# Kernel optimization log

Measured on AMD Instinct MI355X. Metric: run time of the kernel, lower is better.

## Reference

```python
import jax, jax.numpy as jnp
import numpy as np

NHEAD = 4
HEAD_DIM = 64  # att_features per head = atten_feats // nhead


def setup_inputs() -> dict:
    key = jax.random.key(0)
    ks = jax.random.split(key, 8)
    N, D = 8192, 256
    s = 1.0 / np.sqrt(D)
    return {
        "x": jax.random.normal(ks[0], (N, D), dtype=jnp.float32),
        "edge": jax.random.randint(ks[1], (N, N), 0, 2, dtype=jnp.int32),
        "Wq": jax.random.normal(ks[2], (D, D), dtype=jnp.float32) * s,
        "bq": jax.random.normal(ks[3], (D,), dtype=jnp.float32) * 0.01,
        "Wk": jax.random.normal(ks[4], (D, D), dtype=jnp.float32) * s,
        "bk": jax.random.normal(ks[5], (D,), dtype=jnp.float32) * 0.01,
        "Wv": jax.random.normal(ks[6], (D, D), dtype=jnp.float32) * s,
        "bv": jax.random.normal(ks[7], (D,), dtype=jnp.float32) * 0.01,
    }


def _split_heads(t):
    # (N, H*d) -> (H, N, d)
    N = t.shape[0]
    return t.reshape(N, NHEAD, HEAD_DIM).transpose(1, 0, 2)


def reference(x, edge, Wq, bq, Wk, bk, Wv, bv):
    q = _split_heads(x @ Wq + bq)  # (H, N, d)
    k = _split_heads(x @ Wk + bk)
    v = _split_heads(x @ Wv + bv)
    # additive graph mask: 0 where edge.T == 1, -10000 where edge.T == 0
    mask = (edge.T.astype(jnp.float32) - 1.0) * 10000.0  # (N, N)
    scores = jnp.einsum("hnd,hmd->hnm", q, k) / np.sqrt(HEAD_DIM)
    scores = scores + mask[None, :, :]
    attn = jax.nn.softmax(scores, axis=-1)  # dropout is identity at eval
    ctx = jnp.einsum("hnm,hmd->hnd", attn, v)
    # (H, N, d) -> (N, H*d)
    return ctx.transpose(1, 0, 2).reshape(x.shape[0], NHEAD * HEAD_DIM)
```

## Files before the change

### kernel.cpp

```cpp
#include <hip/hip_runtime.h>
#include <stdint.h>

typedef unsigned short u16;
typedef unsigned int u32;
typedef unsigned long long u64;

typedef __attribute__((ext_vector_type(8))) __bf16 bf16x8;
typedef __attribute__((ext_vector_type(4))) float f32x4;

#define NROW 8192
#define DMODEL 256
#define HD 64
#define LDT 72

__device__ __forceinline__ u16 f2bf(float f) {
    u32 u = __builtin_bit_cast(u32, f);
    u += 0x7FFFu + ((u >> 16) & 1u);
    return (u16)(u >> 16);
}
__device__ __forceinline__ bf16x8 ldb8(const u16* p) {
    uint4 v = *(const uint4*)p;
    return __builtin_bit_cast(bf16x8, v);
}
__device__ __forceinline__ f32x4 mfma16(bf16x8 a, bf16x8 b, f32x4 c) {
    return __builtin_amdgcn_mfma_f32_16x16x32_bf16(a, b, c, 0, 0, 0);
}

__global__ __launch_bounds__(256) void k_prep(
    const float* __restrict__ x,
    const float* __restrict__ Wq, const float* __restrict__ Wk,
    const float* __restrict__ Wv,
    u16* __restrict__ xb, u16* __restrict__ Wt) {
    const int t = threadIdx.x;
    if (blockIdx.x < 1024) {
        size_t idx = (size_t)blockIdx.x * 2048 + t * 8;
        f32x4 a = *(const f32x4*)&x[idx];
        f32x4 b = *(const f32x4*)&x[idx + 4];
        uint4 o;
        o.x = (u32)f2bf(a[0]) | ((u32)f2bf(a[1]) << 16);
        o.y = (u32)f2bf(a[2]) | ((u32)f2bf(a[3]) << 16);
        o.z = (u32)f2bf(b[0]) | ((u32)f2bf(b[1]) << 16);
        o.w = (u32)f2bf(b[2]) | ((u32)f2bf(b[3]) << 16);
        *(uint4*)&xb[idx] = o;
        return;
    }
    __shared__ __align__(16) u16 lw[64 * LDT];
    int wb = blockIdx.x - 1024;
    int mat = wb >> 4, tile = wb & 15;
    int k0 = (tile >> 2) * 64, n0 = (tile & 3) * 64;
    const float* W = (mat == 0) ? Wq : ((mat == 1) ? Wk : Wv);
    #pragma unroll
    for (int i = 0; i < 4; ++i) {
        int c = t + 256 * i;
        int k = c >> 4, c4 = c & 15;
        f32x4 w4 = *(const f32x4*)&W[(size_t)(k0 + k) * DMODEL + n0 + c4 * 4];
        uint2 pk;
        pk.x = (u32)f2bf(w4[0]) | ((u32)f2bf(w4[1]) << 16);
        pk.y = (u32)f2bf(w4[2]) | ((u32)f2bf(w4[3]) << 16);
        *(uint2*)&lw[k * LDT + c4 * 4] = pk;
    }
    __syncthreads();
    #pragma unroll
    for (int i = 0; i < 2; ++i) {
        int c = t + 256 * i;
        int n = c >> 3, k8 = c & 7;
        union { uint4 u; u16 s[8]; } pk;
        #pragma unroll
        for (int j = 0; j < 8; ++j) pk.s[j] = lw[(k8 * 8 + j) * LDT + n];
        *(uint4*)&Wt[(size_t)mat * 65536 + (size_t)(n0 + n) * DMODEL + k0 + k8 * 8] = pk.u;
    }
}

__global__ __launch_bounds__(256) void k_bitmask(const int* __restrict__ edge,
                                                 u64* __restrict__ bits) {
    __shared__ u64 lb[8][128];
    const int t = threadIdx.x;
    const int lane = t & 63, w = t >> 6;
    const u32 m8 = blockIdx.x * 8u;
    #pragma unroll
    for (int rr = 0; rr < 2; ++rr) {
        const int mloc = w * 2 + rr;
        const size_t base = (size_t)(m8 + mloc) * NROW;
        for (int nwb = 0; nwb < 128; nwb += 16) {
            int v[16];
            #pragma unroll
            for (int j = 0; j < 16; ++j)
                v[j] = edge[base + (size_t)(nwb + j) * 64 + lane];
            u64 b[16];
            #pragma unroll
            for (int j = 0; j < 16; ++j) b[j] = __ballot(v[j] != 0);
            if (lane == 0) {
                #pragma unroll
                for (int j = 0; j < 16; ++j) lb[mloc][nwb + j] = b[j];
            }
        }
    }
    __syncthreads();
    const int nw = t >> 1, mh = (t & 1) * 4;
    u64 a0 = lb[mh + 0][nw], a1 = lb[mh + 1][nw];
    u64 a2 = lb[mh + 2][nw], a3 = lb[mh + 3][nw];
    u64* dst = &bits[(size_t)nw * NROW + m8 + mh];
    uint4 p0, p1;
    p0.x = (u32)a0; p0.y = (u32)(a0 >> 32); p0.z = (u32)a1; p0.w = (u32)(a1 >> 32);
    p1.x = (u32)a2; p1.y = (u32)(a2 >> 32); p1.z = (u32)a3; p1.w = (u32)(a3 >> 32);
    *(uint4*)dst = p0;
    *(uint4*)(dst + 2) = p1;
}

__global__ __launch_bounds__(256, 3) void k_qkv(
    const u16* __restrict__ xb, const u16* __restrict__ Wt,
    const float* __restrict__ bq, const float* __restrict__ bk,
    const float* __restrict__ bv,
    u16* __restrict__ Qo, u16* __restrict__ Ko, u16* __restrict__ Vt) {
    __shared__ __align__(16) u16 ax[128 * LDT];
    __shared__ __align__(16) u16 wt[64 * LDT];
    const int t = threadIdx.x;
    const int lane = t & 63, wv = t >> 6;
    const int q4 = lane >> 4, l15 = lane & 15;
    const int wr = wv >> 1, wc = wv & 1;
    const int row0 = blockIdx.x * 128;
    const int mat = blockIdx.y >> 2;
    const int c0 = (blockIdx.y & 3) * 64;
    const u16* Wm = Wt + (size_t)mat * 65536;
    const float* bias = (mat == 0) ? bq : ((mat == 1) ? bk : bv);

    f32x4 acc[8];
    #pragma unroll
    for (int i = 0; i < 8; ++i) acc[i] = {0.f, 0.f, 0.f, 0.f};

    for (int kk = 0; kk < DMODEL; kk += 64) {
        #pragma unroll
        for (int i = 0; i < 4; ++i) {
            int c = t + 256 * i;
            int row = c >> 3, c8 = c & 7;
            *(uint4*)&ax[row * LDT + c8 * 8] =
                *(const uint4*)&xb[(size_t)(row0 + row) * DMODEL + kk + c8 * 8];
        }
        #pragma unroll
        for (int i = 0; i < 2; ++i) {
            int c = t + 256 * i;
            int n = c >> 3, c8 = c & 7;
            *(uint4*)&wt[n * LDT + c8 * 8] =
                *(const uint4*)&Wm[(size_t)(c0 + n) * DMODEL + kk + c8 * 8];
        }
        __syncthreads();
        #pragma unroll
        for (int ks = 0; ks < 2; ++ks) {
            bf16x8 xf[4], wf[2];
            #pragma unroll
            for (int it = 0; it < 4; ++it)
                xf[it] = ldb8(&ax[(wr * 64 + it * 16 + l15) * LDT + ks * 32 + q4 * 8]);
            #pragma unroll
            for (int jt = 0; jt < 2; ++jt)
                wf[jt] = ldb8(&wt[(wc * 32 + jt * 16 + l15) * LDT + ks * 32 + q4 * 8]);
            if (mat < 2) {
                #pragma unroll
                for (int it = 0; it < 4; ++it)
                    #pragma unroll
                    for (int jt = 0; jt < 2; ++jt)
                        acc[it * 2 + jt] = mfma16(xf[it], wf[jt], acc[it * 2 + jt]);
            } else {
                #pragma unroll
                for (int jt = 0; jt < 2; ++jt)
                    #pragma unroll
                    for (int it = 0; it < 4; ++it)
                        acc[jt * 4 + it] = mfma16(wf[jt], xf[it], acc[jt * 4 + it]);
            }
        }
        __syncthreads();
    }

    if (mat < 2) {
        u16* out = (mat == 0) ? Qo : Ko;
        const float scale = (mat == 0) ? 0.18033688f : 1.0f;
        #pragma unroll
        for (int jt = 0; jt < 2; ++jt) {
            int col = c0 + wc * 32 + jt * 16 + l15;
            float bcol = bias[col];
            #pragma unroll
            for (int it = 0; it < 4; ++it) {
                int rowb = row0 + wr * 64 + it * 16 + q4 * 4;
                f32x4 a = acc[it * 2 + jt];
                #pragma unroll
                for (int r = 0; r < 4; ++r)
                    out[(size_t)(rowb + r) * DMODEL + col] = f2bf((a[r] + bcol) * scale);
            }
        }
    } else {
        #pragma unroll
        for (int jt = 0; jt < 2; ++jt) {
            #pragma unroll
            for (int r = 0; r < 4; ++r) {
                int drow = c0 + wc * 32 + jt * 16 + q4 * 4 + r;
                float bd = bias[drow];
                #pragma unroll
                for (int it = 0; it < 4; ++it) {
                    int col = row0 + wr * 64 + it * 16 + l15;
                    Vt[(size_t)drow * NROW + col] = f2bf(acc[jt * 4 + it][r] + bd);
                }
            }
        }
    }
}

__global__ __launch_bounds__(256, 3) void k_attn(
    const u16* __restrict__ Q, const u16* __restrict__ K,
    const u16* __restrict__ Vt, const u64* __restrict__ bits,
    float* __restrict__ po) {
    __shared__ __align__(16) u16 sK[2][64 * 64];
    __shared__ __align__(16) u16 sV[2][64 * 64];
    __shared__ __align__(16) u16 sP[4][32 * 64];
    __shared__ __align__(16) u32 sB[2][2][2][64];

    const int t = threadIdx.x;
    const int lane = t & 63, w = t >> 6;
    const int q4 = lane >> 4, l15 = lane & 15;
    const int l7 = l15 & 7;
    const int bid = blockIdx.x;
    const int sl = bid >> 8;
    const int b8 = bid & 255;
    const int h = b8 & 3;
    const int qt = b8 >> 2;
    const int n0 = qt * 128;
    const int mbase = sl * 2048;
    const int half = w >> 1;
    const u32 shift = (u32)((w & 1) * 16 + l15);
    const int sr = t >> 3, sc = t & 7;
    const int ssw = (sc ^ (sr & 7)) * 8;
    const int bg = t >> 6, bm = t & 63;

    bf16x8 qf[2][2];
    #pragma unroll
    for (int nt = 0; nt < 2; ++nt)
        #pragma unroll
        for (int ks = 0; ks < 2; ++ks)
            qf[nt][ks] = ldb8(&Q[(size_t)(n0 + nt * 64 + w * 16 + l15) * DMODEL +
                                 h * HD + ks * 32 + q4 * 8]);

    uint4 onesu = {0x3F803F80u, 0x3F803F80u, 0x3F803F80u, 0x3F803F80u};
    const bf16x8 ones = __builtin_bit_cast(bf16x8, onesu);

    f32x4 o[2][4], lacc[2];
    #pragma unroll
    for (int nt = 0; nt < 2; ++nt) {
        lacc[nt] = {0.f, 0.f, 0.f, 0.f};
        #pragma unroll
        for (int dt = 0; dt < 4; ++dt) o[nt][dt] = {0.f, 0.f, 0.f, 0.f};
    }

    uint4 rk0, rk1, rv0, rv1; uint2 rb;
    {
        rk0 = *(const uint4*)&K[(size_t)(mbase + sr) * DMODEL + h * HD + sc * 8];
        rk1 = *(const uint4*)&K[(size_t)(mbase + 32 + sr) * DMODEL + h * HD + sc * 8];
        rv0 = *(const uint4*)&Vt[(size_t)(h * HD + sr) * NROW + mbase + sc * 8];
        rv1 = *(const uint4*)&Vt[(size_t)(h * HD + 32 + sr) * NROW + mbase + sc * 8];
        if (t < 128) rb = *(const uint2*)&bits[(size_t)(qt * 2 + bg) * NROW + mbase + bm];
        *(uint4*)&sK[0][sr * 64 + ssw] = rk0;
        *(uint4*)&sK[0][(32 + sr) * 64 + ssw] = rk1;
        *(uint4*)&sV[0][sr * 64 + ssw] = rv0;
        *(uint4*)&sV[0][(32 + sr) * 64 + ssw] = rv1;
        if (t < 128) { sB[0][bg][0][bm] = rb.x; sB[0][bg][1][bm] = rb.y; }
    }

    for (int it = 0; it < 32; ++it) {
        __syncthreads();
        const int buf = it & 1;
        if (it < 31) {
            int m0 = mbase + (it + 1) * 64;
            rk0 = *(const uint4*)&K[(size_t)(m0 + sr) * DMODEL + h * HD + sc * 8];
            rk1 = *(const uint4*)&K[(size_t)(m0 + 32 + sr) * DMODEL + h * HD + sc * 8];
            rv0 = *(const uint4*)&Vt[(size_t)(h * HD + sr) * NROW + m0 + sc * 8];
            rv1 = *(const uint4*)&Vt[(size_t)(h * HD + 32 + sr) * NROW + m0 + sc * 8];
            if (t < 128) rb = *(const uint2*)&bits[(size_t)(qt * 2 + bg) * NROW + m0 + bm];
        }

        f32x4 s[2][4];
        #pragma unroll
        for (int nt = 0; nt < 2; ++nt)
            #pragma unroll
            for (int tj = 0; tj < 4; ++tj) s[nt][tj] = {0.f, 0.f, 0.f, 0.f};
        #pragma unroll
        for (int ks = 0; ks < 2; ++ks) {
            bf16x8 kb[4];
            #pragma unroll
            for (int tj = 0; tj < 4; ++tj)
                kb[tj] = ldb8(&sK[buf][(tj * 16 + l15) * 64 + (((ks * 4 + q4) ^ l7) * 8)]);
            #pragma unroll
            for (int nt = 0; nt < 2; ++nt)
                #pragma unroll
                for (int tj = 0; tj < 4; ++tj)
                    s[nt][tj] = mfma16(kb[tj], qf[nt][ks], s[nt][tj]);
        }

        #pragma unroll
        for (int nt = 0; nt < 2; ++nt) {
            #pragma unroll
            for (int tj = 0; tj < 4; ++tj) {
                uint4 bw = *(const uint4*)&sB[buf][nt][half][tj * 16 + q4 * 4];
                u32 wd[4] = {bw.x, bw.y, bw.z, bw.w};
                u32 ub[4];
                #pragma unroll
                for (int r = 0; r < 4; ++r) {
                    float sv = ((wd[r] >> shift) & 1u) ? s[nt][tj][r] : -1e30f;
                    ub[r] = __builtin_bit_cast(u32, __builtin_amdgcn_exp2f(sv));
                }
                uint2 pk;
                pk.x = (ub[0] >> 16) | (ub[1] & 0xFFFF0000u);
                pk.y = (ub[2] >> 16) | (ub[3] & 0xFFFF0000u);
                *(uint2*)&sP[w][(nt * 16 + l15) * 64 +
                                (((tj * 2 + (q4 >> 1)) ^ l7) * 8) + (q4 & 1) * 4] = pk;
            }
        }
        asm volatile("s_waitcnt lgkmcnt(0)" ::: "memory");

        #pragma unroll
        for (int ks = 0; ks < 2; ++ks) {
            bf16x8 pf[2], vb[4];
            #pragma unroll
            for (int nt = 0; nt < 2; ++nt)
                pf[nt] = ldb8(&sP[w][(nt * 16 + l15) * 64 + (((ks * 4 + q4) ^ l7) * 8)]);
            #pragma unroll
            for (int dt = 0; dt < 4; ++dt)
                vb[dt] = ldb8(&sV[buf][(dt * 16 + l15) * 64 + (((ks * 4 + q4) ^ l7) * 8)]);
            #pragma unroll
            for (int nt = 0; nt < 2; ++nt) {
                #pragma unroll
                for (int dt = 0; dt < 4; ++dt)
                    o[nt][dt] = mfma16(pf[nt], vb[dt], o[nt][dt]);
                lacc[nt] = mfma16(pf[nt], ones, lacc[nt]);
            }
        }

        if (it < 31) {
            const int nb = buf ^ 1;
            *(uint4*)&sK[nb][sr * 64 + ssw] = rk0;
            *(uint4*)&sK[nb][(32 + sr) * 64 + ssw] = rk1;
            *(uint4*)&sV[nb][sr * 64 + ssw] = rv0;
            *(uint4*)&sV[nb][(32 + sr) * 64 + ssw] = rv1;
            if (t < 128) { sB[nb][bg][0][bm] = rb.x; sB[nb][bg][1][bm] = rb.y; }
        }
    }

    float* pob = po + (size_t)bid * 8320;
    #pragma unroll
    for (int nt = 0; nt < 2; ++nt)
        #pragma unroll
        for (int dt = 0; dt < 4; ++dt)
            *(f32x4*)&pob[(dt * 16 + l15) * 128 + nt * 64 + w * 16 + q4 * 4] = o[nt][dt];
    if (l15 == 0) {
        #pragma unroll
        for (int nt = 0; nt < 2; ++nt)
            #pragma unroll
            for (int r = 0; r < 4; ++r)
                pob[8192 + nt * 64 + w * 16 + q4 * 4 + r] = lacc[nt][r];
    }
}

__global__ __launch_bounds__(256) void k_reduce(const float* __restrict__ po,
                                                float* __restrict__ out) {
    __shared__ float sT[64 * 132];
    __shared__ float sL[128];
    const int t = threadIdx.x;
    const int b8 = blockIdx.x;
    const int h = b8 & 3;
    const int qt = b8 >> 2;
    const int n0 = qt * 128;
    const size_t base = (size_t)b8 * 8320;
    const int d = t >> 2, ng = (t & 3) * 32;
    f32x4 a[8];
    #pragma unroll
    for (int j = 0; j < 8; ++j) a[j] = {0.f, 0.f, 0.f, 0.f};
    #pragma unroll
    for (int s = 0; s < 4; ++s) {
        const float* p = po + base + (size_t)s * (256 * 8320) + d * 128 + ng;
        #pragma unroll
        for (int j = 0; j < 8; ++j) a[j] += *(const f32x4*)&p[j * 4];
    }
    #pragma unroll
    for (int j = 0; j < 8; ++j) *(f32x4*)&sT[d * 132 + ng + j * 4] = a[j];
    if (t < 128) {
        float l = 0.f;
        #pragma unroll
        for (int s = 0; s < 4; ++s) l += po[base + (size_t)s * (256 * 8320) + 8192 + t];
        sL[t] = l;
    }
    __syncthreads();
    const int n = t >> 1, dg = (t & 1) * 32;
    float inv = __builtin_amdgcn_rcpf(sL[n] + 1e-30f);
    #pragma unroll
    for (int j = 0; j < 8; ++j) {
        f32x4 v;
        #pragma unroll
        for (int i = 0; i < 4; ++i) v[i] = sT[(dg + j * 4 + i) * 132 + n];
        v = v * inv;
        *(f32x4*)&out[(size_t)(n0 + n) * DMODEL + h * HD + dg + j * 4] = v;
    }
}

extern "C" void kernel_launch(void* const* d_in, const int* in_sizes, int n_in,
                              void* d_out, int out_size, void* d_ws, size_t ws_size,
                              hipStream_t stream) {
    const float* x  = (const float*)d_in[0];
    const int* edge = (const int*)d_in[1];
    const float* Wq = (const float*)d_in[2];
    const float* bq = (const float*)d_in[3];
    const float* Wk = (const float*)d_in[4];
    const float* bk = (const float*)d_in[5];
    const float* Wv = (const float*)d_in[6];
    const float* bv = (const float*)d_in[7];

    char* ws = (char*)d_ws;
    u64* bits = (u64*)ws;
    u16* Qo  = (u16*)(ws + (8u << 20));
    u16* Ko  = (u16*)(ws + (12u << 20));
    u16* Vt  = (u16*)(ws + (16u << 20));
    u16* xb  = (u16*)(ws + (20u << 20));
    u16* Wt  = (u16*)(ws + (24u << 20));
    float* po = (float*)(ws + (32u << 20));
    float* out = (float*)d_out;

    hipLaunchKernelGGL(k_prep, dim3(1072), dim3(256), 0, stream, x, Wq, Wk, Wv, xb, Wt);
    hipLaunchKernelGGL(k_bitmask, dim3(1024), dim3(256), 0, stream, edge, bits);
    hipLaunchKernelGGL(k_qkv, dim3(64, 12), dim3(256), 0, stream,
                       xb, Wt, bq, bk, bv, Qo, Ko, Vt);
    hipLaunchKernelGGL(k_attn, dim3(1024), dim3(256), 0, stream, Qo, Ko, Vt, bits, po);
    hipLaunchKernelGGL(k_reduce, dim3(256), dim3(256), 0, stream, po, out);
}
```

Baseline: 503.4 us.

## Merge bitmask into QKV kernel and double attention query tile to 256 rows

The edge-bitmask kernel and the QKV projection kernel are merged into one launch, with the first 1024 blocks building the mask and the rest doing the GEMM, so the two independent jobs can overlap. The attention kernel now processes 256 query rows per block instead of 128, which halves the number of blocks and the re-reads of each K/V tile, and registers, LDS and partial-output size grow to match. Occupancy bound drops to 2 blocks per CU, and the grid falls to 512 blocks on a 256-CU part, which risks lower latency hiding and poorer load balance.

```diff
diff --git a/kernel.cpp b/kernel.cpp
--- a/kernel.cpp
+++ b/kernel.cpp
@@ -71,56 +71,58 @@
     }
 }
 
-__global__ __launch_bounds__(256) void k_bitmask(const int* __restrict__ edge,
-                                                 u64* __restrict__ bits) {
-    __shared__ u64 lb[8][128];
-    const int t = threadIdx.x;
-    const int lane = t & 63, w = t >> 6;
-    const u32 m8 = blockIdx.x * 8u;
-    #pragma unroll
-    for (int rr = 0; rr < 2; ++rr) {
-        const int mloc = w * 2 + rr;
-        const size_t base = (size_t)(m8 + mloc) * NROW;
-        for (int nwb = 0; nwb < 128; nwb += 16) {
-            int v[16];
-            #pragma unroll
-            for (int j = 0; j < 16; ++j)
-                v[j] = edge[base + (size_t)(nwb + j) * 64 + lane];
-            u64 b[16];
-            #pragma unroll
-            for (int j = 0; j < 16; ++j) b[j] = __ballot(v[j] != 0);
-            if (lane == 0) {
-                #pragma unroll
-                for (int j = 0; j < 16; ++j) lb[mloc][nwb + j] = b[j];
-            }
-        }
-    }
-    __syncthreads();
-    const int nw = t >> 1, mh = (t & 1) * 4;
-    u64 a0 = lb[mh + 0][nw], a1 = lb[mh + 1][nw];
-    u64 a2 = lb[mh + 2][nw], a3 = lb[mh + 3][nw];
-    u64* dst = &bits[(size_t)nw * NROW + m8 + mh];
-    uint4 p0, p1;
-    p0.x = (u32)a0; p0.y = (u32)(a0 >> 32); p0.z = (u32)a1; p0.w = (u32)(a1 >> 32);
-    p1.x = (u32)a2; p1.y = (u32)(a2 >> 32); p1.z = (u32)a3; p1.w = (u32)(a3 >> 32);
-    *(uint4*)dst = p0;
-    *(uint4*)(dst + 2) = p1;
-}
-
-__global__ __launch_bounds__(256, 3) void k_qkv(
+__global__ __launch_bounds__(256, 3) void k_qkvmask(
+    const int* __restrict__ edge, u64* __restrict__ bits,
     const u16* __restrict__ xb, const u16* __restrict__ Wt,
     const float* __restrict__ bq, const float* __restrict__ bk,
     const float* __restrict__ bv,
     u16* __restrict__ Qo, u16* __restrict__ Ko, u16* __restrict__ Vt) {
     __shared__ __align__(16) u16 ax[128 * LDT];
     __shared__ __align__(16) u16 wt[64 * LDT];
+    __shared__ u64 lb[8][128];
     const int t = threadIdx.x;
     const int lane = t & 63, wv = t >> 6;
+
+    if (blockIdx.x < 1024) {
+        const u32 m8 = blockIdx.x * 8u;
+        #pragma unroll
+        for (int rr = 0; rr < 2; ++rr) {
+            const int mloc = wv * 2 + rr;
+            const size_t base = (size_t)(m8 + mloc) * NROW;
+            for (int nwb = 0; nwb < 128; nwb += 16) {
+                int v[16];
+                #pragma unroll
+                for (int j = 0; j < 16; ++j)
+                    v[j] = edge[base + (size_t)(nwb + j) * 64 + lane];
+                u64 b[16];
+                #pragma unroll
+                for (int j = 0; j < 16; ++j) b[j] = __ballot(v[j] != 0);
+                if (lane == 0) {
+                    #pragma unroll
+                    for (int j = 0; j < 16; ++j) lb[mloc][nwb + j] = b[j];
+                }
+            }
+        }
+        __syncthreads();
+        const int nw = t >> 1, mh = (t & 1) * 4;
+        u64 a0 = lb[mh + 0][nw], a1 = lb[mh + 1][nw];
+        u64 a2 = lb[mh + 2][nw], a3 = lb[mh + 3][nw];
+        u64* dst = &bits[(size_t)nw * NROW + m8 + mh];
+        uint4 p0, p1;
+        p0.x = (u32)a0; p0.y = (u32)(a0 >> 32); p0.z = (u32)a1; p0.w = (u32)(a1 >> 32);
+        p1.x = (u32)a2; p1.y = (u32)(a2 >> 32); p1.z = (u32)a3; p1.w = (u32)(a3 >> 32);
+        *(uint4*)dst = p0;
+        *(uint4*)(dst + 2) = p1;
+        return;
+    }
+
+    const int q = blockIdx.x - 1024;
     const int q4 = lane >> 4, l15 = lane & 15;
     const int wr = wv >> 1, wc = wv & 1;
-    const int row0 = blockIdx.x * 128;
-    const int mat = blockIdx.y >> 2;
-    const int c0 = (blockIdx.y & 3) * 64;
+    const int row0 = (q & 63) * 128;
+    const int ymat = q >> 6;
+    const int mat = ymat >> 2;
+    const int c0 = (ymat & 3) * 64;
     const u16* Wm = Wt + (size_t)mat * 65536;
     const float* bias = (mat == 0) ? bq : ((mat == 1) ? bk : bv);
 
@@ -203,25 +205,25 @@
     }
 }
 
-__global__ __launch_bounds__(256, 3) void k_attn(
+__global__ __launch_bounds__(256, 2) void k_attn(
     const u16* __restrict__ Q, const u16* __restrict__ K,
     const u16* __restrict__ Vt, const u64* __restrict__ bits,
     float* __restrict__ po) {
     __shared__ __align__(16) u16 sK[2][64 * 64];
     __shared__ __align__(16) u16 sV[2][64 * 64];
-    __shared__ __align__(16) u16 sP[4][32 * 64];
-    __shared__ __align__(16) u32 sB[2][2][2][64];
+    __shared__ __align__(16) u16 sP[4][64 * 64];
+    __shared__ __align__(16) u32 sB[2][4][2][64];
 
     const int t = threadIdx.x;
     const int lane = t & 63, w = t >> 6;
     const int q4 = lane >> 4, l15 = lane & 15;
     const int l7 = l15 & 7;
     const int bid = blockIdx.x;
-    const int sl = bid >> 8;
-    const int b8 = bid & 255;
-    const int h = b8 & 3;
-    const int qt = b8 >> 2;
-    const int n0 = qt * 128;
+    const int sl = bid >> 7;
+    const int b7 = bid & 127;
+    const int h = b7 & 3;
+    const int qt = b7 >> 2;
+    const int n0 = qt * 256;
     const int mbase = sl * 2048;
     const int half = w >> 1;
     const u32 shift = (u32)((w & 1) * 16 + l15);
@@ -229,9 +231,9 @@
     const int ssw = (sc ^ (sr & 7)) * 8;
     const int bg = t >> 6, bm = t & 63;
 
-    bf16x8 qf[2][2];
-    #pragma unroll
-    for (int nt = 0; nt < 2; ++nt)
+    bf16x8 qf[4][2];
+    #pragma unroll
+    for (int nt = 0; nt < 4; ++nt)
         #pragma unroll
         for (int ks = 0; ks < 2; ++ks)
             qf[nt][ks] = ldb8(&Q[(size_t)(n0 + nt * 64 + w * 16 + l15) * DMODEL +
@@ -240,9 +242,9 @@
     uint4 onesu = {0x3F803F80u, 0x3F803F80u, 0x3F803F80u, 0x3F803F80u};
     const bf16x8 ones = __builtin_bit_cast(bf16x8, onesu);
 
-    f32x4 o[2][4], lacc[2];
-    #pragma unroll
-    for (int nt = 0; nt < 2; ++nt) {
+    f32x4 o[4][4], lacc[4];
+    #pragma unroll
+    for (int nt = 0; nt < 4; ++nt) {
         lacc[nt] = {0.f, 0.f, 0.f, 0.f};
         #pragma unroll
         for (int dt = 0; dt < 4; ++dt) o[nt][dt] = {0.f, 0.f, 0.f, 0.f};
@@ -254,12 +256,12 @@
         rk1 = *(const uint4*)&K[(size_t)(mbase + 32 + sr) * DMODEL + h * HD + sc * 8];
         rv0 = *(const uint4*)&Vt[(size_t)(h * HD + sr) * NROW + mbase + sc * 8];
         rv1 = *(const uint4*)&Vt[(size_t)(h * HD + 32 + sr) * NROW + mbase + sc * 8];
-        if (t < 128) rb = *(const uint2*)&bits[(size_t)(qt * 2 + bg) * NROW + mbase + bm];
+        rb = *(const uint2*)&bits[(size_t)(qt * 4 + bg) * NROW + mbase + bm];
         *(uint4*)&sK[0][sr * 64 + ssw] = rk0;
         *(uint4*)&sK[0][(32 + sr) * 64 + ssw] = rk1;
         *(uint4*)&sV[0][sr * 64 + ssw] = rv0;
         *(uint4*)&sV[0][(32 + sr) * 64 + ssw] = rv1;
-        if (t < 128) { sB[0][bg][0][bm] = rb.x; sB[0][bg][1][bm] = rb.y; }
+        sB[0][bg][0][bm] = rb.x; sB[0][bg][1][bm] = rb.y;
     }
 
     for (int it = 0; it < 32; ++it) {
@@ -271,29 +273,26 @@
             rk1 = *(const uint4*)&K[(size_t)(m0 + 32 + sr) * DMODEL + h * HD + sc * 8];
             rv0 = *(const uint4*)&Vt[(size_t)(h * HD + sr) * NROW + m0 + sc * 8];
             rv1 = *(const uint4*)&Vt[(size_t)(h * HD + 32 + sr) * NROW + m0 + sc * 8];
-            if (t < 128) rb = *(const uint2*)&bits[(size_t)(qt * 2 + bg) * NROW + m0 + bm];
-        }
-
-        f32x4 s[2][4];
-        #pragma unroll
-        for (int nt = 0; nt < 2; ++nt)
-            #pragma unroll
-            for (int tj = 0; tj < 4; ++tj) s[nt][tj] = {0.f, 0.f, 0.f, 0.f};
-        #pragma unroll
-        for (int ks = 0; ks < 2; ++ks) {
-            bf16x8 kb[4];
+            rb = *(const uint2*)&bits[(size_t)(qt * 4 + bg) * NROW + m0 + bm];
+        }
+
+        bf16x8 kb[2][4];
+        #pragma unroll
+        for (int ks = 0; ks < 2; ++ks)
             #pragma unroll
             for (int tj = 0; tj < 4; ++tj)
-                kb[tj] = ldb8(&sK[buf][(tj * 16 + l15) * 64 + (((ks * 4 + q4) ^ l7) * 8)]);
-            #pragma unroll
-            for (int nt = 0; nt < 2; ++nt)
+                kb[ks][tj] = ldb8(&sK[buf][(tj * 16 + l15) * 64 + (((ks * 4 + q4) ^ l7) * 8)]);
+
+        #pragma unroll
+        for (int nt = 0; nt < 4; ++nt) {
+            f32x4 s[4];
+            #pragma unroll
+            for (int tj = 0; tj < 4; ++tj) s[tj] = {0.f, 0.f, 0.f, 0.f};
+            #pragma unroll
+            for (int ks = 0; ks < 2; ++ks)
                 #pragma unroll
                 for (int tj = 0; tj < 4; ++tj)
-                    s[nt][tj] = mfma16(kb[tj], qf[nt][ks], s[nt][tj]);
-        }
-
-        #pragma unroll
-        for (int nt = 0; nt < 2; ++nt) {
+                    s[tj] = mfma16(kb[ks][tj], qf[nt][ks], s[tj]);
             #pragma unroll
             for (int tj = 0; tj < 4; ++tj) {
                 uint4 bw = *(const uint4*)&sB[buf][nt][half][tj * 16 + q4 * 4];
@@ -301,7 +300,7 @@
                 u32 ub[4];
                 #pragma unroll
                 for (int r = 0; r < 4; ++r) {
-                    float sv = ((wd[r] >> shift) & 1u) ? s[nt][tj][r] : -1e30f;
+                    float sv = ((wd[r] >> shift) & 1u) ? s[tj][r] : -1e30f;
                     ub[r] = __builtin_bit_cast(u32, __builtin_amdgcn_exp2f(sv));
                 }
                 uint2 pk;
@@ -315,19 +314,17 @@
 
         #pragma unroll
         for (int ks = 0; ks < 2; ++ks) {
-            bf16x8 pf[2], vb[4];
-            #pragma unroll
-            for (int nt = 0; nt < 2; ++nt)
-                pf[nt] = ldb8(&sP[w][(nt * 16 + l15) * 64 + (((ks * 4 + q4) ^ l7) * 8)]);
+            bf16x8 vb[4];
             #pragma unroll
             for (int dt = 0; dt < 4; ++dt)
                 vb[dt] = ldb8(&sV[buf][(dt * 16 + l15) * 64 + (((ks * 4 + q4) ^ l7) * 8)]);
             #pragma unroll
-            for (int nt = 0; nt < 2; ++nt) {
+            for (int nt = 0; nt < 4; ++nt) {
+                bf16x8 pf = ldb8(&sP[w][(nt * 16 + l15) * 64 + (((ks * 4 + q4) ^ l7) * 8)]);
                 #pragma unroll
                 for (int dt = 0; dt < 4; ++dt)
-                    o[nt][dt] = mfma16(pf[nt], vb[dt], o[nt][dt]);
-                lacc[nt] = mfma16(pf[nt], ones, lacc[nt]);
+                    o[nt][dt] = mfma16(pf, vb[dt], o[nt][dt]);
+                lacc[nt] = mfma16(pf, ones, lacc[nt]);
             }
         }
 
@@ -337,63 +334,63 @@
             *(uint4*)&sK[nb][(32 + sr) * 64 + ssw] = rk1;
             *(uint4*)&sV[nb][sr * 64 + ssw] = rv0;
             *(uint4*)&sV[nb][(32 + sr) * 64 + ssw] = rv1;
-            if (t < 128) { sB[nb][bg][0][bm] = rb.x; sB[nb][bg][1][bm] = rb.y; }
-        }
-    }
-
-    float* pob = po + (size_t)bid * 8320;
-    #pragma unroll
-    for (int nt = 0; nt < 2; ++nt)
+            sB[nb][bg][0][bm] = rb.x; sB[nb][bg][1][bm] = rb.y;
+        }
+    }
+
+    float* pob = po + (size_t)bid * 16640;
+    #pragma unroll
+    for (int nt = 0; nt < 4; ++nt)
         #pragma unroll
         for (int dt = 0; dt < 4; ++dt)
-            *(f32x4*)&pob[(dt * 16 + l15) * 128 + nt * 64 + w * 16 + q4 * 4] = o[nt][dt];
+            *(f32x4*)&pob[(dt * 16 + l15) * 256 + nt * 64 + w * 16 + q4 * 4] = o[nt][dt];
     if (l15 == 0) {
         #pragma unroll
-        for (int nt = 0; nt < 2; ++nt)
+        for (int nt = 0; nt < 4; ++nt)
             #pragma unroll
             for (int r = 0; r < 4; ++r)
-                pob[8192 + nt * 64 + w * 16 + q4 * 4 + r] = lacc[nt][r];
+                pob[16384 + nt * 64 + w * 16 + q4 * 4 + r] = lacc[nt][r];
     }
 }
 
 __global__ __launch_bounds__(256) void k_reduce(const float* __restrict__ po,
                                                 float* __restrict__ out) {
-    __shared__ float sT[64 * 132];
-    __shared__ float sL[128];
+    __shared__ float sT[64 * 260];
+    __shared__ float sL[256];
     const int t = threadIdx.x;
-    const int b8 = blockIdx.x;
-    const int h = b8 & 3;
-    const int qt = b8 >> 2;
-    const int n0 = qt * 128;
-    const size_t base = (size_t)b8 * 8320;
-    const int d = t >> 2, ng = (t & 3) * 32;
-    f32x4 a[8];
-    #pragma unroll
-    for (int j = 0; j < 8; ++j) a[j] = {0.f, 0.f, 0.f, 0.f};
+    const int b = blockIdx.x;
+    const int h = b & 3;
+    const int qt = b >> 2;
+    const int n0 = qt * 256;
+    const size_t base = (size_t)b * 16640;
+    const int d = t >> 2, ng = (t & 3) * 64;
+    f32x4 a[16];
+    #pragma unroll
+    for (int j = 0; j < 16; ++j) a[j] = {0.f, 0.f, 0.f, 0.f};
     #pragma unroll
     for (int s = 0; s < 4; ++s) {
-        const float* p = po + base + (size_t)s * (256 * 8320) + d * 128 + ng;
-        #pragma unroll
-        for (int j = 0; j < 8; ++j) a[j] += *(const f32x4*)&p[j * 4];
-    }
-    #pragma unroll
-    for (int j = 0; j < 8; ++j) *(f32x4*)&sT[d * 132 + ng + j * 4] = a[j];
-    if (t < 128) {
+        const float* p = po + base + (size_t)s * (128 * 16640) + d * 256 + ng;
+        #pragma unroll
+        for (int j = 0; j < 16; ++j) a[j] += *(const f32x4*)&p[j * 4];
+    }
+    #pragma unroll
+    for (int j = 0; j < 16; ++j) *(f32x4*)&sT[d * 260 + ng + j * 4] = a[j];
+    {
         float l = 0.f;
         #pragma unroll
-        for (int s = 0; s < 4; ++s) l += po[base + (size_t)s * (256 * 8320) + 8192 + t];
+        for (int s = 0; s < 4; ++s) l += po[base + (size_t)s * (128 * 16640) + 16384 + t];
         sL[t] = l;
     }
     __syncthreads();
-    const int n = t >> 1, dg = (t & 1) * 32;
+    const int n = t;
     float inv = __builtin_amdgcn_rcpf(sL[n] + 1e-30f);
     #pragma unroll
-    for (int j = 0; j < 8; ++j) {
+    for (int j = 0; j < 16; ++j) {
         f32x4 v;
         #pragma unroll
-        for (int i = 0; i < 4; ++i) v[i] = sT[(dg + j * 4 + i) * 132 + n];
+        for (int i = 0; i < 4; ++i) v[i] = sT[(j * 4 + i) * 260 + n];
         v = v * inv;
-        *(f32x4*)&out[(size_t)(n0 + n) * DMODEL + h * HD + dg + j * 4] = v;
+        *(f32x4*)&out[(size_t)(n0 + n) * DMODEL + h * HD + j * 4] = v;
     }
 }
 
@@ -420,9 +417,8 @@
     float* out = (float*)d_out;
 
     hipLaunchKernelGGL(k_prep, dim3(1072), dim3(256), 0, stream, x, Wq, Wk, Wv, xb, Wt);
-    hipLaunchKernelGGL(k_bitmask, dim3(1024), dim3(256), 0, stream, edge, bits);
-    hipLaunchKernelGGL(k_qkv, dim3(64, 12), dim3(256), 0, stream,
-                       xb, Wt, bq, bk, bv, Qo, Ko, Vt);
-    hipLaunchKernelGGL(k_attn, dim3(1024), dim3(256), 0, stream, Qo, Ko, Vt, bits, po);
-    hipLaunchKernelGGL(k_reduce, dim3(256), dim3(256), 0, stream, po, out);
-}
+    hipLaunchKernelGGL(k_qkvmask, dim3(1792), dim3(256), 0, stream,
+                       edge, bits, xb, Wt, bq, bk, bv, Qo, Ko, Vt);
+    hipLaunchKernelGGL(k_attn, dim3(512), dim3(256), 0, stream, Qo, Ko, Vt, bits, po);
+    hipLaunchKernelGGL(k_reduce, dim3(128), dim3(256), 0, stream, po, out);
+}
```

Result: no change. 507.5 us (+0.8%).
